# Kernel tuning notes

Hardware: AMD Instinct MI355X
Metric: run time of the kernel (lower is better)

## Reference

```python
import jax, jax.numpy as jnp
import numpy as np
from math import factorial, pi, sqrt

N_ATOMS = 4096
N_PAIRS = 49152
F = 16           # num_tensordense_features
NUM_RADIAL = 16  # basis num=16
NUM_SPECIES = 95
EMB_DIM = 32
CUTOFF = 5.0
LMAX = 4         # SelfAttention max_degree=4
NLM = 25
LMAX_B = 2       # basis max_degree=2 (also max_tensordense_degree)
NLM_B = 9

DEG9 = np.repeat(np.arange(3), [1, 3, 5])        # degree index of each lm, l<=2
DEG25 = np.repeat(np.arange(5), [1, 3, 5, 7, 9]) # degree index of each lm, l<=4


def real_sph(u, lmax):
    # real spherical harmonics (m = -l..l ordering, no Condon-Shortley), u: (...,3) unit vectors
    x, y, z = u[..., 0], u[..., 1], u[..., 2]
    phi = jnp.arctan2(y, x)
    ct = jnp.clip(z, -1.0, 1.0)
    st = jnp.sqrt(jnp.clip(1.0 - ct * ct, 0.0, 1.0))
    P = {(0, 0): jnp.ones_like(ct)}
    for m in range(1, lmax + 1):
        P[(m, m)] = -(2 * m - 1) * st * P[(m - 1, m - 1)]
    for m in range(0, lmax):
        P[(m + 1, m)] = (2 * m + 1) * ct * P[(m, m)]
    for m in range(0, lmax + 1):
        for l in range(m + 2, lmax + 1):
            P[(l, m)] = ((2 * l - 1) * ct * P[(l - 1, m)] - (l + m - 1) * P[(l - 2, m)]) / (l - m)
    outs = []
    for l in range(lmax + 1):
        for m in range(-l, l + 1):
            ma = abs(m)
            Nn = sqrt((2 * l + 1) / (4 * pi) * factorial(l - ma) / factorial(l + ma))
            cs = (-1.0) ** ma  # cancel Condon-Shortley in P
            if m == 0:
                Y = Nn * P[(l, 0)]
            elif m > 0:
                Y = sqrt(2.0) * Nn * cs * jnp.cos(m * phi) * P[(l, m)]
            else:
                Y = sqrt(2.0) * Nn * cs * jnp.sin(ma * phi) * P[(l, ma)]
            outs.append(Y)
    return jnp.stack(outs, axis=-1)


def _gaunt():
    # exact real Gaunt (CG-equivalent) coupling coefficients via Gauss-Legendre x uniform-phi quadrature
    nt, nph = 16, 32
    xs, ws = np.polynomial.legendre.leggauss(nt)
    phis = np.arange(nph) * (2 * np.pi / nph)
    ct = np.repeat(xs, nph); ph = np.tile(phis, nt)
    st = np.sqrt(np.clip(1.0 - ct ** 2, 0.0, 1.0))
    u = np.stack([st * np.cos(ph), st * np.sin(ph), ct], -1)
    w = np.repeat(ws, nph) * (2 * np.pi / nph)
    Y = np.asarray(real_sph(jnp.asarray(u, dtype=jnp.float32), LMAX))
    G = np.einsum('gi,gj,gk,g->ijk', Y, Y[:, :NLM_B], Y, w)
    G[np.abs(G) < 1e-6] = 0.0
    return G

_G = _gaunt()
G_ATT = jnp.asarray(_G, dtype=jnp.float32)                      # (25, 9, 25): feat x basis -> feat
G_TD = jnp.asarray(_G[:NLM_B, :, :NLM_B], dtype=jnp.float32)    # (9, 9, 9): TensorDense coupling


def pdense(x, W, deg):
    return jnp.einsum('plf,lfg->plg', x, W[deg])


def couple(xf, Bf, G):
    # equivariant tensor product  out[p,k,f] = sum_ij G[i,j,k] xf[p,i,f] Bf[p,j,f]
    u = jnp.einsum('pif,ijk->pjkf', xf, G)
    return jnp.einsum('pjf,pjkf->pkf', Bf, u)


def setup_inputs() -> dict:
    key = jax.random.key(0)
    ks = jax.random.split(key, 24)
    s = 1.0 / np.sqrt(F)
    inp = dict(
        atomic_numbers=jax.random.randint(ks[0], (N_ATOMS,), 0, NUM_SPECIES),
        neighbour_indices=jnp.stack([
            jax.random.randint(ks[1], (N_PAIRS,), 0, N_ATOMS),
            jax.random.randint(ks[2], (N_PAIRS,), 0, N_ATOMS)], axis=-1),
        neighbour_displacements=jax.random.normal(ks[3], (N_PAIRS, 3), dtype=jnp.float32) * 1.7,
        W_rad=jax.random.normal(ks[4], (NUM_SPECIES, NUM_RADIAL, F), dtype=jnp.float32) / np.sqrt(NUM_RADIAL),
        emb_table=jax.random.normal(ks[5], (NUM_SPECIES, EMB_DIM), dtype=jnp.float32),
        W_emb=jax.random.normal(ks[6], (EMB_DIM, F), dtype=jnp.float32) / np.sqrt(EMB_DIM),
        b_emb=jnp.zeros((F,), jnp.float32),
        td_W1=jax.random.normal(ks[7], (3, F, F), dtype=jnp.float32) * s,
        td_W2=jax.random.normal(ks[8], (3, F, F), dtype=jnp.float32) * s,
        td_W3=jax.random.normal(ks[9], (3, F, F), dtype=jnp.float32) * s,
        Wb1=jax.random.normal(ks[10], (NUM_RADIAL, F), dtype=jnp.float32) / np.sqrt(NUM_RADIAL),
        Wq1=jax.random.normal(ks[11], (5, F, F), dtype=jnp.float32) * s,
        Wk1=jax.random.normal(ks[12], (5, F, F), dtype=jnp.float32) * s,
        Wv1=jax.random.normal(ks[13], (5, F, F), dtype=jnp.float32) * s,
        Wo1=jax.random.normal(ks[14], (5, F, F), dtype=jnp.float32) * s,
        bo1=jnp.zeros((F,), jnp.float32),
        Wb2=jax.random.normal(ks[15], (NUM_RADIAL, F), dtype=jnp.float32) / np.sqrt(NUM_RADIAL),
        Wq2=jax.random.normal(ks[16], (5, F, F), dtype=jnp.float32) * s,
        Wk2=jax.random.normal(ks[17], (5, F, F), dtype=jnp.float32) * s,
        Wv2=jax.random.normal(ks[18], (5, F, F), dtype=jnp.float32) * s,
        Wo2=jax.random.normal(ks[19], (5, F, F), dtype=jnp.float32) * s,
        bo2=jnp.zeros((F,), jnp.float32),
    )
    return inp


def reference(atomic_numbers, neighbour_indices, neighbour_displacements,
              W_rad, emb_table, W_emb, b_emb, td_W1, td_W2, td_W3,
              Wb1, Wq1, Wk1, Wv1, Wo1, bo1, Wb2, Wq2, Wk2, Wv2, Wo2, bo2):
    dst = neighbour_indices[:, 0]   # idx_i
    src = neighbour_indices[:, 1]   # idx_j
    Zj = atomic_numbers[src]
    r = jnp.linalg.norm(neighbour_displacements, axis=-1)
    u = neighbour_displacements / jnp.maximum(r, 1e-9)[:, None]
    sh = real_sph(u, LMAX)          # (P, 25)
    sh_b = sh[:, :NLM_B]            # (P, 9)
    kk = jnp.arange(1, NUM_RADIAL + 1, dtype=jnp.float32)
    rb = jnp.sinc(kk[None, :] * r[:, None] / CUTOFF) * (r < CUTOFF)[:, None]  # sinc basis w/ cutoff
    # species-aware radial basis -> per-pair equivariant features (P, 9, F)
    y0 = jnp.einsum('pk,pkf->pf', rb, W_rad[Zj])
    y = sh_b[:, :, None] * y0[:, None, :]
    # TensorDense: dense -> CG tensor product -> dense (degrees <= 2)
    a = pdense(y, td_W1, DEG9)
    b = pdense(y, td_W2, DEG9)
    u9 = jnp.einsum('pif,ijk->pjkf', a, G_TD)
    tp = jnp.einsum('pjf,pjkf->pkf', b, u9)
    y = pdense(tp, td_W3, DEG9)
    # aggregate per-pair messages to atoms (segment mean), pad degrees to l<=4
    sums = jnp.zeros((N_ATOMS, NLM_B, F), y.dtype).at[dst].add(y)
    cnt = jnp.zeros((N_ATOMS,), y.dtype).at[dst].add(1.0)
    x = sums / jnp.maximum(cnt, 1.0)[:, None, None]
    x = jnp.pad(x, ((0, 0), (0, NLM - NLM_B), (0, 0)))  # (N, 25, F)
    # two segment self-attention layers over neighbour pairs
    for (Wb, Wq, Wk, Wv, Wo, bo) in ((Wb1, Wq1, Wk1, Wv1, Wo1, bo1), (Wb2, Wq2, Wk2, Wv2, Wo2, bo2)):
        Bf = sh_b[:, :, None] * (rb @ Wb)[:, None, :]   # projected pair basis (P, 9, F)
        q = pdense(x, Wq, DEG25)[dst]
        kf = couple(pdense(x, Wk, DEG25)[src], Bf, G_ATT)
        vf = couple(pdense(x, Wv, DEG25)[src], Bf, G_ATT)
        s = jnp.einsum('plf,plf->p', q, kf) / np.sqrt(NLM * F)
        m = jax.lax.stop_gradient(jnp.full((N_ATOMS,), -1e30, s.dtype).at[dst].max(s))
        e = jnp.exp(s - m[dst])
        den = jnp.zeros((N_ATOMS,), s.dtype).at[dst].add(e)
        alpha = e / (den[dst] + 1e-9)
        agg = jnp.zeros((N_ATOMS, NLM, F), x.dtype).at[dst].add(alpha[:, None, None] * vf)
        x = pdense(agg, Wo, DEG25)
        x = x.at[:, 0, :].add(bo)
    # embedding residual connection on the scalar (l=0) channel
    res = emb_table[atomic_numbers] @ W_emb + b_emb
    x = x.at[:, 0, :].add(res)
    return x
```

## Files before the change

### kernel.cpp

```cpp
#include <hip/hip_runtime.h>
#include <hip/hip_bf16.h>

#define NA 4096
#define NP 49152

typedef _Float16 f16;
typedef _Float16 h2 __attribute__((ext_vector_type(2)));
union U4H { uint4 u; f16 h[8]; h2 p[4]; };

__device__ __forceinline__ float fdot2(h2 a, h2 b, float c){
#if __has_builtin(__builtin_amdgcn_fdot2)
  return __builtin_amdgcn_fdot2(a, b, c, false);
#else
  return c + (float)a.x*(float)b.x + (float)a.y*(float)b.y;
#endif
}

constexpr int WS_Y     = 0;
constexpr int WS_G     = 12800;
constexpr int WS_NATT  = WS_G + 5632;
constexpr int WS_ATTW  = WS_NATT + 8;
constexpr int WS_ATTIJ = WS_ATTW + 1024;
constexpr int WS_TDOFS = WS_ATTIJ + 1024;
constexpr int WS_TDW   = WS_TDOFS + 16;
constexpr int WS_TDIJ  = WS_TDW + 512;
constexpr int WS_AOFS  = WS_TDIJ + 512;
constexpr int WS_SH    = WS_AOFS + 32;
constexpr int WS_RB    = WS_SH + NP*9;
constexpr int WS_S     = WS_RB + NP*16;
constexpr int WS_CCNT  = WS_S + NP;
constexpr int WS_COFF  = WS_CCNT + NA;
constexpr int WS_CCUR  = WS_COFF + NA + 8;
constexpr int WS_CLST  = WS_CCUR + NA;
constexpr int WS_XQ    = WS_CLST + NP;
constexpr int WS_XK    = WS_XQ + NA*400;
constexpr int WS_XV    = WS_XK + NA*400;
constexpr int WS_PVF   = WS_XV + NA*400;
constexpr int WS_WW    = WS_PVF + NP*128;
constexpr long long WS_END = (long long)WS_PVF + (long long)NP*256;

__device__ const float  GLX[16] = {
  -0.98940093499164993f, -0.94457502307323258f, -0.86563120238783174f, -0.75540440835500303f,
  -0.61787624440264375f, -0.45801677765722739f, -0.28160355077925891f, -0.09501250983763744f,
   0.09501250983763744f,  0.28160355077925891f,  0.45801677765722739f,  0.61787624440264375f,
   0.75540440835500303f,  0.86563120238783174f,  0.94457502307323258f,  0.98940093499164993f };
__device__ const double GLW[16] = {
  0.02715245941175409, 0.06225352393864789, 0.09515851168249278, 0.12462897125553387,
  0.14959598881657673, 0.16915651939500254, 0.18260341504492359, 0.18945061045506850,
  0.18945061045506850, 0.18260341504492359, 0.16915651939500254, 0.14959598881657673,
  0.12462897125553387, 0.09515851168249278, 0.06225352393864789, 0.02715245941175409 };

#define PI_D 3.14159265358979323846

__device__ __forceinline__ float scrub(float v){
  if(!(v == v)) return 0.f;
  return fminf(fmaxf(v, -1e30f), 1e30f);
}

__device__ void real_sph25(float ct, float phi, float* Y){
  float st = sqrtf(fmaxf(0.f, 1.f - ct*ct));
  float P[5][5];
  P[0][0] = 1.f;
  #pragma unroll
  for(int m=1;m<=4;m++) P[m][m] = -(2.f*m - 1.f)*st*P[m-1][m-1];
  #pragma unroll
  for(int m=0;m<4;m++) P[m+1][m] = (2.f*m + 1.f)*ct*P[m][m];
  #pragma unroll
  for(int m=0;m<=4;m++){
    #pragma unroll
    for(int l=m+2;l<=4;l++)
      P[l][m] = ((2.f*l - 1.f)*ct*P[l-1][m] - (float)(l+m-1)*P[l-2][m]) / (float)(l-m);
  }
  const double fact[9] = {1,1,2,6,24,120,720,5040,40320};
  int idx = 0;
  #pragma unroll
  for(int l=0;l<=4;l++){
    #pragma unroll
    for(int m=-l;m<=l;m++){
      int ma = (m < 0) ? -m : m;
      float Nn = (float)sqrt((2*l+1)/(4.0*PI_D)*fact[l-ma]/fact[l+ma]);
      float cs = (ma & 1) ? -1.f : 1.f;
      float v;
      if(m == 0)      v = Nn * P[l][0];
      else if(m > 0)  v = 1.4142135623730951f * Nn * cs * cosf(ma*phi) * P[l][ma];
      else            v = 1.4142135623730951f * Nn * cs * sinf(ma*phi) * P[l][ma];
      Y[idx++] = v;
    }
  }
}

__global__ __launch_bounds__(256) void kq_G(float* ws){
  __shared__ float Ysh[12800];
  int tid = threadIdx.x;
  for(int pt=tid; pt<512; pt+=256){
    float ct  = GLX[pt >> 5];
    float phi = (float)((pt & 31) * (2.0*PI_D/32.0));
    float Y[25];
    real_sph25(ct, phi, Y);
    #pragma unroll
    for(int i=0;i<25;i++) Ysh[pt*25 + i] = Y[i];
  }
  __syncthreads();
  int idx = blockIdx.x*256 + tid;
  int t = idx >> 3, chunk = idx & 7;
  if(t >= 5625) return;
  int k = t % 25, j = (t/25) % 9, i = t/225;
  double acc = 0.0;
  int g0 = chunk*64;
  #pragma unroll 4
  for(int g=g0; g<g0+64; g++){
    double w = GLW[g >> 5] * (2.0*PI_D/32.0);
    acc += w * (double)Ysh[g*25+i] * (double)Ysh[g*25+j] * (double)Ysh[g*25+k];
  }
  acc += __shfl_xor(acc, 1, 8);
  acc += __shfl_xor(acc, 2, 8);
  acc += __shfl_xor(acc, 4, 8);
  if(chunk == 0){
    if(fabs(acc) < 1e-6) acc = 0.0;
    ws[WS_G + (i*9+j)*25 + k] = (float)acc;
  }
}

__global__ __launch_bounds__(64) void kq_lists(float* ws){
  __shared__ float Gsh[5632];
  __shared__ int cA[25], cT[9], oA[26], oT[10];
  int t = threadIdx.x;
  for(int i=t; i<5625; i+=64) Gsh[i] = ws[WS_G + i];
  __syncthreads();
  const float* G = Gsh;
  if(t < 25){ int c=0; for(int i=0;i<25;i++) for(int j=0;j<9;j++) if(G[(i*9+j)*25+t] != 0.f) c++; cA[t]=c; }
  if(t < 9){  int c=0; for(int i=0;i<9;i++)  for(int j=0;j<9;j++) if(G[(i*9+j)*25+t] != 0.f) c++; cT[t]=c; }
  __syncthreads();
  if(t == 0){
    int s=0; for(int k=0;k<25;k++){ oA[k]=s; s+=cA[k]; } oA[25]=s;
    ((int*)ws)[WS_NATT] = s;
    s=0; for(int k=0;k<9;k++){ oT[k]=s; s+=cT[k]; } oT[9]=s;
  }
  __syncthreads();
  float* attw = ws + WS_ATTW; int* attij = (int*)ws + WS_ATTIJ;
  int* aofs = (int*)ws + WS_AOFS;
  if(t < 26) aofs[t] = oA[t] < 1024 ? oA[t] : 1024;
  if(t < 25){
    int pos = oA[t];
    for(int i=0;i<25;i++) for(int j=0;j<9;j++){
      float w = G[(i*9+j)*25+t];
      if(w != 0.f && pos < 1024){ attw[pos]=w; attij[pos] = i | (j<<5) | (t<<9); pos++; }
    }
  }
  float* tdw = ws + WS_TDW; int* tdij = (int*)ws + WS_TDIJ; int* tdofs = (int*)ws + WS_TDOFS;
  if(t < 9){
    int pos = oT[t];
    for(int i=0;i<9;i++) for(int j=0;j<9;j++){
      float w = G[(i*9+j)*25+t];
      if(w != 0.f && pos < 512){
        int li = (i==0)?0:(i<4)?1:2, lj = (j==0)?0:(j<4)?1:2;
        tdw[pos]=w; tdij[pos] = i | (j<<5) | (li<<10) | (lj<<12); pos++;
      }
    }
    tdofs[t] = oT[t];
    if(t == 0) tdofs[9] = oT[9];
  }
}

__global__ void k_pair(const float* disp, const int* nbr, float* ws){
  int p = blockIdx.x*256 + threadIdx.x;
  if(p >= NP) return;
  float dx = disp[3*p], dy = disp[3*p+1], dz = disp[3*p+2];
  float r = sqrtf(dx*dx + dy*dy + dz*dz);
  float inv = 1.f / fmaxf(r, 1e-9f);
  float ux = dx*inv, uy = dy*inv, uz = dz*inv;
  float sh[9];
  sh[0] = 0.28209479177387814f;
  sh[1] = 0.4886025119029199f * uy;
  sh[2] = 0.4886025119029199f * uz;
  sh[3] = 0.4886025119029199f * ux;
  sh[4] = 1.0925484305920792f * ux*uy;
  sh[5] = 1.0925484305920792f * uy*uz;
  sh[6] = 0.31539156525252005f * (3.f*uz*uz - 1.f);
  sh[7] = 1.0925484305920792f * ux*uz;
  sh[8] = 0.5462742152960396f * (ux*ux - uy*uy);
  #pragma unroll
  for(int i=0;i<9;i++) ws[WS_SH + p*9 + i] = scrub(sh[i]);
  float mask = (r < 5.f) ? 1.f : 0.f;
  #pragma unroll
  for(int k=1;k<=16;k++){
    float x  = (float)k * r * 0.2f;
    float px = 3.14159265358979323846f * x;
    float s  = (px < 1e-6f) ? 1.f : (sinf(px)/px);
    ws[WS_RB + p*16 + (k-1)] = scrub(s * mask);
  }
  atomicAdd((int*)ws + WS_CCNT + nbr[2*p], 1);
}

__global__ __launch_bounds__(1024) void k_scan(float* ws){
  __shared__ int part[1024];
  int t = threadIdx.x;
  const int* cnt = (const int*)ws + WS_CCNT;
  int v0 = cnt[4*t], v1 = cnt[4*t+1], v2 = cnt[4*t+2], v3 = cnt[4*t+3];
  part[t] = v0+v1+v2+v3;
  __syncthreads();
  for(int o=1; o<1024; o<<=1){
    int x = (t >= o) ? part[t-o] : 0;
    __syncthreads();
    part[t] += x;
    __syncthreads();
  }
  int base = (t > 0) ? part[t-1] : 0;
  int* offp = (int*)ws + WS_COFF;
  int* cur  = (int*)ws + WS_CCUR;
  offp[4*t]   = base;          cur[4*t]   = base;
  offp[4*t+1] = base+v0;       cur[4*t+1] = base+v0;
  offp[4*t+2] = base+v0+v1;    cur[4*t+2] = base+v0+v1;
  offp[4*t+3] = base+v0+v1+v2; cur[4*t+3] = base+v0+v1+v2;
  if(t == 1023) offp[4096] = part[1023];
}

__global__ void k_fill(const int* nbr, float* ws){
  int p = blockIdx.x*256 + threadIdx.x;
  if(p >= NP) return;
  int d = nbr[2*p];
  int pos = atomicAdd((int*)ws + WS_CCUR + d, 1);
  ((int*)ws)[WS_CLST + pos] = p;
}

__global__ __launch_bounds__(256) void k_ww(const float* Wrad, const float* W1,
                                            const float* W2, float* ws){
  int s = blockIdx.x;
  #pragma unroll
  for(int it=0; it<6; it++){
    int idx = threadIdx.x + 256*it;
    int w = idx / 768, r = idx % 768;
    int d = r / 256, r2 = r % 256, k = r2 / 16, g = r2 % 16;
    const float* Wsrc = (w == 0) ? W1 : W2;
    float acc = 0.f;
    #pragma unroll
    for(int fp=0; fp<16; fp++)
      acc += Wrad[(s*16+k)*16+fp] * Wsrc[(d*16+fp)*16+g];
    ws[WS_WW + ((size_t)(s*2+w)*16 + g)*48 + d*16 + k] = acc;
  }
}

__global__ __launch_bounds__(256) void k_td(const int* aZ, const int* nbr,
    const float* W3, float* ws){
  __shared__ float sh_s[16][9];
  __shared__ float S_s[16][88];
  __shared__ float tp_s[16][9][16];
  int tid = threadIdx.x, pl = tid >> 4, g = tid & 15;
  int sp = blockIdx.x*16 + pl;
  int p = ((const int*)ws)[WS_CLST + sp];
  int src = nbr[2*p+1];
  int Zj = aZ[src];
  {
    float4* S4 = (float4*)&S_s[0][0];
    for(int t0=tid; t0<352; t0+=256) S4[t0] = make_float4(0.f,0.f,0.f,0.f);
  }
  if(g < 9) sh_s[pl][g] = ws[WS_SH + p*9 + g];
  float rb[16];
  {
    const float4* rb4 = (const float4*)(ws + WS_RB + p*16);
    #pragma unroll
    for(int c=0;c<4;c++){
      float4 r = rb4[c];
      rb[4*c]=r.x; rb[4*c+1]=r.y; rb[4*c+2]=r.z; rb[4*c+3]=r.w;
    }
  }
  float A1[3], A2[3];
  {
    const float4* w1 = (const float4*)(ws + WS_WW + ((size_t)(Zj*2+0)*16+g)*48);
    const float4* w2 = (const float4*)(ws + WS_WW + ((size_t)(Zj*2+1)*16+g)*48);
    #pragma unroll
    for(int d=0; d<3; d++){
      float a1 = 0.f, a2 = 0.f;
      #pragma unroll
      for(int c=0;c<4;c++){
        float4 x1 = w1[d*4+c], x2 = w2[d*4+c];
        a1 += x1.x*rb[4*c] + x1.y*rb[4*c+1] + x1.z*rb[4*c+2] + x1.w*rb[4*c+3];
        a2 += x2.x*rb[4*c] + x2.y*rb[4*c+1] + x2.z*rb[4*c+2] + x2.w*rb[4*c+3];
      }
      A1[d] = a1; A2[d] = a2;
    }
  }
  __syncthreads();
  if(g < 9){
    const float* tdw = ws + WS_TDW;
    const int* tdij  = (const int*)ws + WS_TDIJ;
    const int* tdofs = (const int*)ws + WS_TDOFS;
    int e1 = tdofs[g+1];
    for(int e=tdofs[g]; e<e1; e++){
      float w = tdw[e]; int meta = tdij[e];
      int i = meta & 31, j = (meta>>5) & 15, li = (meta>>10) & 3, lj = (meta>>12) & 3;
      S_s[pl][g*9 + li*3 + lj] += w * sh_s[pl][i] * sh_s[pl][j];
    }
  }
  __syncthreads();
  float AA[9];
  #pragma unroll
  for(int li=0;li<3;li++)
    #pragma unroll
    for(int lj=0;lj<3;lj++) AA[li*3+lj] = A1[li]*A2[lj];
  #pragma unroll
  for(int k=0;k<9;k++){
    float tpv = 0.f;
    #pragma unroll
    for(int c=0;c<9;c++) tpv += S_s[pl][k*9+c] * AA[c];
    tp_s[pl][k][g] = tpv;
  }
  __syncthreads();
  float w3r[48];
  #pragma unroll
  for(int d=0;d<3;d++)
    #pragma unroll
    for(int f2=0;f2<16;f2++) w3r[d*16+f2] = W3[(d*16+f2)*16+g];
  float acc9[9];
  #pragma unroll
  for(int k=0;k<9;k++){
    int d = (k==0)?0:(k<4)?1:2;
    const float4* t4 = (const float4*)&tp_s[pl][k][0];
    float acc = 0.f;
    #pragma unroll
    for(int c=0;c<4;c++){
      float4 t = t4[c];
      acc += t.x*w3r[d*16+4*c] + t.y*w3r[d*16+4*c+1] + t.z*w3r[d*16+4*c+2] + t.w*w3r[d*16+4*c+3];
    }
    acc9[k] = scrub(acc);
  }
  f16* ptd = (f16*)(ws + WS_PVF) + (size_t)sp*256 + g*16;
  U4H u0, u1;
  #pragma unroll
  for(int j=0;j<8;j++) u0.h[j] = (f16)acc9[j];
  u1.h[0] = (f16)acc9[8];
  #pragma unroll
  for(int j=1;j<8;j++) u1.h[j] = (f16)0.f;
  *(uint4*)(ptd)     = u0.u;
  *(uint4*)(ptd + 8) = u1.u;
}

__global__ __launch_bounds__(256) void k_tdq(const float* Wq, const float* Wk,
                                             const float* Wv, float* ws){
  __shared__ float xsh[4][144];
  __shared__ float wq_sh[768], wk_sh[768], wv_sh[768];
  int tid = threadIdx.x, al = tid >> 6, lane = tid & 63;
  int a = blockIdx.x*4 + al;
  for(int t=tid; t<768; t+=256){ wq_sh[t]=Wq[t]; wk_sh[t]=Wk[t]; wv_sh[t]=Wv[t]; }
  const int* coff = (const int*)ws + WS_COFF;
  int off0 = coff[a], n = coff[a+1] - off0;
  const f16* base = (const f16*)(ws + WS_PVF);
  float acc[8] = {0,0,0,0,0,0,0,0};
  if(lane < 32){
    for(int t=0; t<n; t++){
      U4H u; u.u = *(const uint4*)(base + (size_t)(off0+t)*256 + lane*8);
      #pragma unroll
      for(int j=0;j<8;j++) acc[j] += (float)u.h[j];
    }
  }
  float invn = 1.f / fmaxf((float)n, 1.f);
  if(lane < 32){
    int gg = lane >> 1;
    #pragma unroll
    for(int j=0;j<8;j++){
      int k = (lane & 1)*8 + j;
      if(k < 9) xsh[al][k*16 + gg] = scrub(acc[j]*invn);
    }
  }
  __syncthreads();
  int g = lane & 15, q4 = lane >> 4;
  f16* qt = (f16*)(ws + WS_XQ) + (size_t)a*800 + g*32;
  f16* kt = (f16*)(ws + WS_XK) + (size_t)a*800 + g*32;
  f16* vt = (f16*)(ws + WS_XV) + (size_t)a*800 + g*32;
  for(int i=q4; i<9; i+=4){
    int l = (i==0)?0:(i<4)?1:2;
    float q=0.f, k2=0.f, v2=0.f;
    #pragma unroll
    for(int f2=0;f2<16;f2++){
      float xv = xsh[al][i*16+f2];
      q  += xv*wq_sh[(l*16+f2)*16+g];
      k2 += xv*wk_sh[(l*16+f2)*16+g];
      v2 += xv*wv_sh[(l*16+f2)*16+g];
    }
    qt[i] = (f16)q; kt[i] = (f16)k2; vt[i] = (f16)v2;
  }
}

template<int NI>
__global__ __launch_bounds__(128) void k_att(const int* nbr, const float* Wb, float* ws){
  __shared__ __align__(16) f16 Ml[8][840];
  __shared__ float sh_s[8][9];
  constexpr int NPAIR = NI/2;
  constexpr int TAIL  = NI-1;
  int tid = threadIdx.x, pl = tid >> 4, g = tid & 15;
  int sp = blockIdx.x*8 + pl;
  int p = ((const int*)ws)[WS_CLST + sp];
  {
    uint4 z; z.x=0; z.y=0; z.z=0; z.w=0;
    uint4* Mz = (uint4*)&Ml[0][0];
    for(int t0=tid; t0<840; t0+=128) Mz[t0] = z;
  }
  if(g < 9) sh_s[pl][g] = ws[WS_SH + p*9 + g];
  float wbreg[16];
  #pragma unroll
  for(int k=0;k<16;k++) wbreg[k] = Wb[k*16+g];
  __syncthreads();
  {
    const float* attw = ws + WS_ATTW;
    const int* attij  = (const int*)ws + WS_ATTIJ;
    const int* aofs   = (const int*)ws + WS_AOFS;
    for(int kr=g; kr<25; kr+=16){
      f16* Mrow = &Ml[pl][kr*32];
      int e = aofs[kr], e1 = aofs[kr+1];
      int meta = attij[e];
      int curi = meta & 31;
      float cur = 0.f;
      for(; e<e1; e++){
        meta = attij[e];
        int i2 = meta & 31;
        if(i2 != curi){ Mrow[curi] = (f16)cur; cur = 0.f; curi = i2; }
        cur += attw[e] * sh_s[pl][(meta>>5) & 15];
      }
      Mrow[curi] = (f16)cur;
    }
  }
  __syncthreads();
  int dst = nbr[2*p], src = nbr[2*p+1];
  float q_r[NI];
  {
    const f16* qt = (const f16*)(ws + WS_XQ) + (size_t)dst*800 + g*32;
    #pragma unroll
    for(int c=0;c<NPAIR/4;c++){
      U4H u; u.u = *(const uint4*)(qt + c*8);
      #pragma unroll
      for(int j=0;j<8;j++) q_r[c*8+j] = (float)u.h[j];
    }
    q_r[TAIL] = (float)qt[TAIL];
  }
  h2 xk2[NPAIR], xv2[NPAIR];
  float xkT, xvT;
  {
    const f16* kt = (const f16*)(ws + WS_XK) + (size_t)src*800 + g*32;
    const f16* vt = (const f16*)(ws + WS_XV) + (size_t)src*800 + g*32;
    #pragma unroll
    for(int c=0;c<NPAIR/4;c++){
      U4H uk; uk.u = *(const uint4*)(kt + c*8);
      U4H uv; uv.u = *(const uint4*)(vt + c*8);
      #pragma unroll
      for(int j=0;j<4;j++){ xk2[c*4+j] = uk.p[j]; xv2[c*4+j] = uv.p[j]; }
    }
    xkT = (float)kt[TAIL];
    xvT = (float)vt[TAIL];
  }
  float wbf;
  {
    const float4* rb4 = (const float4*)(ws + WS_RB + p*16);
    float acc = 0.f;
    #pragma unroll
    for(int c=0;c<4;c++){
      float4 r = rb4[c];
      acc += r.x*wbreg[4*c] + r.y*wbreg[4*c+1] + r.z*wbreg[4*c+2] + r.w*wbreg[4*c+3];
    }
    wbf = acc;
  }
  f16* pvf = (f16*)(ws + WS_PVF) + (size_t)sp*400;
  float sacc = 0.f;
  #pragma unroll
  for(int k=0;k<25;k++){
    const uint4* Mq = (const uint4*)&Ml[pl][k*32];
    float mT = (float)Ml[pl][k*32 + TAIL];
    float vv = 0.f, kf = 0.f;
    #pragma unroll
    for(int c=0;c<NPAIR/4;c++){
      U4H u; u.u = Mq[c];
      #pragma unroll
      for(int j=0;j<4;j++){
        vv = fdot2(u.p[j], xv2[c*4+j], vv);
        if(k < NI) kf = fdot2(u.p[j], xk2[c*4+j], kf);
      }
    }
    vv += mT * xvT;
    if(k < NI){
      kf += mT * xkT;
      sacc += q_r[k]*kf;
    }
    pvf[k*16 + g] = (f16)scrub(wbf*vv);
  }
  float sl = sacc;
  #pragma unroll
  for(int off=1; off<16; off<<=1) sl += __shfl_xor(sl, off, 16);
  if(g == 0) ws[WS_S + sp] = scrub(sl * 0.05f);
}

template<bool FINAL>
__global__ __launch_bounds__(256) void k_aggo(const float* Wo, const float* bo,
    const int* aZ, const float* emb, const float* Wemb, const float* bemb,
    const float* Wq, const float* Wk, const float* Wv, float* ws, float* out){
  __shared__ float xsh[4][400];
  __shared__ float wo_sh[1280];
  __shared__ float wq_sh[FINAL?4:1280], wk_sh[FINAL?4:1280], wv_sh[FINAL?4:1280];
  __shared__ float osh[FINAL?4:1600];
  int tid = threadIdx.x, al = tid >> 6, lane = tid & 63;
  int a = blockIdx.x*4 + al;
  for(int t=tid; t<1280; t+=256){
    wo_sh[t] = Wo[t];
    if(!FINAL){ wq_sh[t]=Wq[t]; wk_sh[t]=Wk[t]; wv_sh[t]=Wv[t]; }
  }
  const int* coff = (const int*)ws + WS_COFF;
  int off0 = coff[a], n = coff[a+1] - off0;
  float mx = -1e30f;
  for(int t=lane; t<n; t+=64) mx = fmaxf(mx, ws[WS_S + off0 + t]);
  #pragma unroll
  for(int off=1; off<64; off<<=1) mx = fmaxf(mx, __shfl_xor(mx, off));
  float den = 0.f;
  for(int t=lane; t<n; t+=64) den += expf(fminf(ws[WS_S + off0 + t] - mx, 0.f));
  #pragma unroll
  for(int off=1; off<64; off<<=1) den += __shfl_xor(den, off);
  float inv_den = 1.f / (den + 1e-9f);
  float acc[8] = {0,0,0,0,0,0,0,0};
  const f16* base = (const f16*)(ws + WS_PVF);
  for(int t=0; t<n; t++){
    float alpha = expf(fminf(ws[WS_S + off0 + t] - mx, 0.f)) * inv_den;
    if(lane < 50){
      U4H u; u.u = *(const uint4*)(base + (size_t)(off0+t)*400 + lane*8);
      #pragma unroll
      for(int j=0;j<8;j++) acc[j] += alpha * (float)u.h[j];
    }
  }
  if(lane < 50){
    #pragma unroll
    for(int j=0;j<8;j++) xsh[al][lane*8 + j] = scrub(acc[j]);
  }
  __syncthreads();
  int g = lane & 15, q4 = lane >> 4;
  for(int i=q4; i<25; i+=4){
    int l = (i==0)?0:(i<4)?1:(i<9)?2:(i<16)?3:4;
    float accv = 0.f;
    #pragma unroll
    for(int f2=0;f2<16;f2++) accv += xsh[al][i*16+f2]*wo_sh[(l*16+f2)*16+g];
    if(i == 0){
      accv += bo[g];
      if(FINAL){
        int Z = aZ[a];
        float res = bemb[g];
        #pragma unroll
        for(int e2=0;e2<32;e2++) res += emb[Z*32+e2]*Wemb[e2*16+g];
        accv += res;
      }
    }
    if(FINAL) out[a*400 + i*16 + g] = scrub(accv);
    else      osh[al*400 + i*16 + g] = scrub(accv);
  }
  if(!FINAL){
    __syncthreads();
    f16* qt = (f16*)(ws + WS_XQ) + (size_t)a*800 + g*32;
    f16* kt = (f16*)(ws + WS_XK) + (size_t)a*800 + g*32;
    f16* vt = (f16*)(ws + WS_XV) + (size_t)a*800 + g*32;
    for(int i=q4; i<25; i+=4){
      int l = (i==0)?0:(i<4)?1:(i<9)?2:(i<16)?3:4;
      float q=0.f, k2=0.f, v2=0.f;
      #pragma unroll
      for(int f2=0;f2<16;f2++){
        float xv = osh[al*400 + i*16 + f2];
        q  += xv*wq_sh[(l*16+f2)*16+g];
        k2 += xv*wk_sh[(l*16+f2)*16+g];
        v2 += xv*wv_sh[(l*16+f2)*16+g];
      }
      qt[i] = (f16)q; kt[i] = (f16)k2; vt[i] = (f16)v2;
    }
  }
}

extern "C" void kernel_launch(void* const* d_in, const int* in_sizes, int n_in,
                              void* d_out, int out_size, void* d_ws, size_t ws_size,
                              hipStream_t stream){
  (void)in_sizes; (void)n_in; (void)out_size;
  if(ws_size < (size_t)WS_END * sizeof(float)) return;
  float* ws = (float*)d_ws;
  const int* aZ  = (const int*)d_in[0];
  const int* nbr = (const int*)d_in[1];
  const float* disp = (const float*)d_in[2];
  const float* Wrad = (const float*)d_in[3];
  const float* emb  = (const float*)d_in[4];
  const float* Wemb = (const float*)d_in[5];
  const float* bemb = (const float*)d_in[6];
  const float* W1   = (const float*)d_in[7];
  const float* W2   = (const float*)d_in[8];
  const float* W3   = (const float*)d_in[9];
  const float* Wb1 = (const float*)d_in[10]; const float* Wq1 = (const float*)d_in[11];
  const float* Wk1 = (const float*)d_in[12]; const float* Wv1 = (const float*)d_in[13];
  const float* Wo1 = (const float*)d_in[14]; const float* bo1 = (const float*)d_in[15];
  const float* Wb2 = (const float*)d_in[16]; const float* Wq2 = (const float*)d_in[17];
  const float* Wk2 = (const float*)d_in[18]; const float* Wv2 = (const float*)d_in[19];
  const float* Wo2 = (const float*)d_in[20]; const float* bo2 = (const float*)d_in[21];

  kq_G<<<176,256,0,stream>>>(ws);
  kq_lists<<<1,64,0,stream>>>(ws);
  hipMemsetAsync(ws + WS_CCNT, 0, NA*sizeof(int), stream);
  k_pair<<<192,256,0,stream>>>(disp, nbr, ws);
  k_scan<<<1,1024,0,stream>>>(ws);
  k_fill<<<192,256,0,stream>>>(nbr, ws);
  k_ww<<<95,256,0,stream>>>(Wrad, W1, W2, ws);
  k_td<<<3072,256,0,stream>>>(aZ, nbr, W3, ws);
  k_tdq<<<1024,256,0,stream>>>(Wq1, Wk1, Wv1, ws);

  k_att<9><<<6144,128,0,stream>>>(nbr, Wb1, ws);
  k_aggo<false><<<1024,256,0,stream>>>(Wo1, bo1, aZ, emb, Wemb, bemb,
                                       Wq2, Wk2, Wv2, ws, nullptr);
  k_att<25><<<6144,128,0,stream>>>(nbr, Wb2, ws);
  k_aggo<true><<<1024,256,0,stream>>>(Wo2, bo2, aZ, emb, Wemb, bemb,
                                      nullptr, nullptr, nullptr, ws, (float*)d_out);
}
```

Measured before the change: 427.2 us.

## Store pair data in dst-sorted order and trim layer-1 attention coupling lists

Pair counting is split out of k_pair so the sorted pair order exists before spherical harmonics and radial basis are written. Those values, plus dst/src indices, are then stored at the sorted position, so k_td and k_att read contiguously instead of indirecting through the pair list and the neighbour array. A separate coupling list restricted to i<9 is built for the first attention layer, with a smaller shared-memory M tile. Wb is staged through shared memory instead of per-thread registers. This adds one extra kernel launch and an inverse-index scatter in k_fill.

```diff
diff --git a/kernel.cpp b/kernel.cpp
--- a/kernel.cpp
+++ b/kernel.cpp
@@ -16,7 +16,9 @@
 #endif
 }
 
-constexpr int WS_Y     = 0;
+constexpr int WS_AOFS9 = 64;
+constexpr int WS_ATTW9 = 128;
+constexpr int WS_ATTIJ9= WS_ATTW9 + 512;
 constexpr int WS_G     = 12800;
 constexpr int WS_NATT  = WS_G + 5632;
 constexpr int WS_ATTW  = WS_NATT + 8;
@@ -37,7 +39,10 @@
 constexpr int WS_XV    = WS_XK + NA*400;
 constexpr int WS_PVF   = WS_XV + NA*400;
 constexpr int WS_WW    = WS_PVF + NP*128;
-constexpr long long WS_END = (long long)WS_PVF + (long long)NP*256;
+constexpr int WS_PVFE  = WS_PVF + NP*256;
+constexpr int WS_INV   = WS_PVFE;
+constexpr int WS_DS    = WS_INV + NP;
+constexpr long long WS_END = (long long)WS_DS + 2*NP + 16;
 
 __device__ const float  GLX[16] = {
   -0.98940093499164993f, -0.94457502307323258f, -0.86563120238783174f, -0.75540440835500303f,
@@ -123,28 +128,38 @@
 
 __global__ __launch_bounds__(64) void kq_lists(float* ws){
   __shared__ float Gsh[5632];
-  __shared__ int cA[25], cT[9], oA[26], oT[10];
+  __shared__ int cA[25], cT[9], cA9[25], oA[26], oT[10], oA9[26];
   int t = threadIdx.x;
   for(int i=t; i<5625; i+=64) Gsh[i] = ws[WS_G + i];
   __syncthreads();
   const float* G = Gsh;
-  if(t < 25){ int c=0; for(int i=0;i<25;i++) for(int j=0;j<9;j++) if(G[(i*9+j)*25+t] != 0.f) c++; cA[t]=c; }
+  if(t < 25){
+    int c=0, c9=0;
+    for(int i=0;i<25;i++) for(int j=0;j<9;j++) if(G[(i*9+j)*25+t] != 0.f){ c++; if(i<9) c9++; }
+    cA[t]=c; cA9[t]=c9;
+  }
   if(t < 9){  int c=0; for(int i=0;i<9;i++)  for(int j=0;j<9;j++) if(G[(i*9+j)*25+t] != 0.f) c++; cT[t]=c; }
   __syncthreads();
   if(t == 0){
     int s=0; for(int k=0;k<25;k++){ oA[k]=s; s+=cA[k]; } oA[25]=s;
     ((int*)ws)[WS_NATT] = s;
+    s=0; for(int k=0;k<25;k++){ oA9[k]=s; s+=cA9[k]; } oA9[25]=s;
     s=0; for(int k=0;k<9;k++){ oT[k]=s; s+=cT[k]; } oT[9]=s;
   }
   __syncthreads();
-  float* attw = ws + WS_ATTW; int* attij = (int*)ws + WS_ATTIJ;
-  int* aofs = (int*)ws + WS_AOFS;
-  if(t < 26) aofs[t] = oA[t] < 1024 ? oA[t] : 1024;
+  float* attw = ws + WS_ATTW;  int* attij = (int*)ws + WS_ATTIJ;
+  float* attw9 = ws + WS_ATTW9; int* attij9 = (int*)ws + WS_ATTIJ9;
+  int* aofs  = (int*)ws + WS_AOFS;
+  int* aofs9 = (int*)ws + WS_AOFS9;
+  if(t < 26){ aofs[t] = oA[t] < 1024 ? oA[t] : 1024; aofs9[t] = oA9[t] < 512 ? oA9[t] : 512; }
   if(t < 25){
-    int pos = oA[t];
+    int pos = oA[t], pos9 = oA9[t];
     for(int i=0;i<25;i++) for(int j=0;j<9;j++){
       float w = G[(i*9+j)*25+t];
-      if(w != 0.f && pos < 1024){ attw[pos]=w; attij[pos] = i | (j<<5) | (t<<9); pos++; }
+      if(w != 0.f){
+        if(pos < 1024){ attw[pos]=w; attij[pos] = i | (j<<5) | (t<<9); pos++; }
+        if(i < 9 && pos9 < 512){ attw9[pos9]=w; attij9[pos9] = i | (j<<5) | (t<<9); pos9++; }
+      }
     }
   }
   float* tdw = ws + WS_TDW; int* tdij = (int*)ws + WS_TDIJ; int* tdofs = (int*)ws + WS_TDOFS;
@@ -162,9 +177,50 @@
   }
 }
 
-__global__ void k_pair(const float* disp, const int* nbr, float* ws){
+__global__ void k_cnt(const int* nbr, float* ws){
   int p = blockIdx.x*256 + threadIdx.x;
   if(p >= NP) return;
+  atomicAdd((int*)ws + WS_CCNT + nbr[2*p], 1);
+}
+
+__global__ __launch_bounds__(1024) void k_scan(float* ws){
+  __shared__ int part[1024];
+  int t = threadIdx.x;
+  const int* cnt = (const int*)ws + WS_CCNT;
+  int v0 = cnt[4*t], v1 = cnt[4*t+1], v2 = cnt[4*t+2], v3 = cnt[4*t+3];
+  part[t] = v0+v1+v2+v3;
+  __syncthreads();
+  for(int o=1; o<1024; o<<=1){
+    int x = (t >= o) ? part[t-o] : 0;
+    __syncthreads();
+    part[t] += x;
+    __syncthreads();
+  }
+  int base = (t > 0) ? part[t-1] : 0;
+  int* offp = (int*)ws + WS_COFF;
+  int* cur  = (int*)ws + WS_CCUR;
+  offp[4*t]   = base;          cur[4*t]   = base;
+  offp[4*t+1] = base+v0;       cur[4*t+1] = base+v0;
+  offp[4*t+2] = base+v0+v1;    cur[4*t+2] = base+v0+v1;
+  offp[4*t+3] = base+v0+v1+v2; cur[4*t+3] = base+v0+v1+v2;
+  if(t == 1023) offp[4096] = part[1023];
+}
+
+__global__ void k_fill(const int* nbr, float* ws){
+  int p = blockIdx.x*256 + threadIdx.x;
+  if(p >= NP) return;
+  int d = nbr[2*p], s = nbr[2*p+1];
+  int pos = atomicAdd((int*)ws + WS_CCUR + d, 1);
+  ((int*)ws)[WS_CLST + pos] = p;
+  ((int*)ws)[WS_INV + p] = pos;
+  ((int*)ws)[WS_DS + 2*pos]     = d;
+  ((int*)ws)[WS_DS + 2*pos + 1] = s;
+}
+
+__global__ void k_pair(const float* disp, float* ws){
+  int p = blockIdx.x*256 + threadIdx.x;
+  if(p >= NP) return;
+  int sp = ((const int*)ws)[WS_INV + p];
   float dx = disp[3*p], dy = disp[3*p+1], dz = disp[3*p+2];
   float r = sqrtf(dx*dx + dy*dy + dz*dz);
   float inv = 1.f / fmaxf(r, 1e-9f);
@@ -180,47 +236,19 @@
   sh[7] = 1.0925484305920792f * ux*uz;
   sh[8] = 0.5462742152960396f * (ux*ux - uy*uy);
   #pragma unroll
-  for(int i=0;i<9;i++) ws[WS_SH + p*9 + i] = scrub(sh[i]);
+  for(int i=0;i<9;i++) ws[WS_SH + sp*9 + i] = scrub(sh[i]);
   float mask = (r < 5.f) ? 1.f : 0.f;
+  float rbv[16];
   #pragma unroll
   for(int k=1;k<=16;k++){
     float x  = (float)k * r * 0.2f;
     float px = 3.14159265358979323846f * x;
     float s  = (px < 1e-6f) ? 1.f : (sinf(px)/px);
-    ws[WS_RB + p*16 + (k-1)] = scrub(s * mask);
-  }
-  atomicAdd((int*)ws + WS_CCNT + nbr[2*p], 1);
-}
-
-__global__ __launch_bounds__(1024) void k_scan(float* ws){
-  __shared__ int part[1024];
-  int t = threadIdx.x;
-  const int* cnt = (const int*)ws + WS_CCNT;
-  int v0 = cnt[4*t], v1 = cnt[4*t+1], v2 = cnt[4*t+2], v3 = cnt[4*t+3];
-  part[t] = v0+v1+v2+v3;
-  __syncthreads();
-  for(int o=1; o<1024; o<<=1){
-    int x = (t >= o) ? part[t-o] : 0;
-    __syncthreads();
-    part[t] += x;
-    __syncthreads();
-  }
-  int base = (t > 0) ? part[t-1] : 0;
-  int* offp = (int*)ws + WS_COFF;
-  int* cur  = (int*)ws + WS_CCUR;
-  offp[4*t]   = base;          cur[4*t]   = base;
-  offp[4*t+1] = base+v0;       cur[4*t+1] = base+v0;
-  offp[4*t+2] = base+v0+v1;    cur[4*t+2] = base+v0+v1;
-  offp[4*t+3] = base+v0+v1+v2; cur[4*t+3] = base+v0+v1+v2;
-  if(t == 1023) offp[4096] = part[1023];
-}
-
-__global__ void k_fill(const int* nbr, float* ws){
-  int p = blockIdx.x*256 + threadIdx.x;
-  if(p >= NP) return;
-  int d = nbr[2*p];
-  int pos = atomicAdd((int*)ws + WS_CCUR + d, 1);
-  ((int*)ws)[WS_CLST + pos] = p;
+    rbv[k-1] = scrub(s * mask);
+  }
+  float4* rb4 = (float4*)(ws + WS_RB + sp*16);
+  #pragma unroll
+  for(int c=0;c<4;c++) rb4[c] = make_float4(rbv[4*c], rbv[4*c+1], rbv[4*c+2], rbv[4*c+3]);
 }
 
 __global__ __launch_bounds__(256) void k_ww(const float* Wrad, const float* W1,
@@ -240,24 +268,22 @@
   }
 }
 
-__global__ __launch_bounds__(256) void k_td(const int* aZ, const int* nbr,
-    const float* W3, float* ws){
+__global__ __launch_bounds__(256) void k_td(const int* aZ, const float* W3, float* ws){
   __shared__ float sh_s[16][9];
   __shared__ float S_s[16][88];
   __shared__ float tp_s[16][9][16];
   int tid = threadIdx.x, pl = tid >> 4, g = tid & 15;
   int sp = blockIdx.x*16 + pl;
-  int p = ((const int*)ws)[WS_CLST + sp];
-  int src = nbr[2*p+1];
+  int src = ((const int*)ws)[WS_DS + 2*sp + 1];
   int Zj = aZ[src];
   {
     float4* S4 = (float4*)&S_s[0][0];
     for(int t0=tid; t0<352; t0+=256) S4[t0] = make_float4(0.f,0.f,0.f,0.f);
   }
-  if(g < 9) sh_s[pl][g] = ws[WS_SH + p*9 + g];
+  if(g < 9) sh_s[pl][g] = ws[WS_SH + sp*9 + g];
   float rb[16];
   {
-    const float4* rb4 = (const float4*)(ws + WS_RB + p*16);
+    const float4* rb4 = (const float4*)(ws + WS_RB + sp*16);
     #pragma unroll
     for(int c=0;c<4;c++){
       float4 r = rb4[c];
@@ -382,45 +408,48 @@
 }
 
 template<int NI>
-__global__ __launch_bounds__(128) void k_att(const int* nbr, const float* Wb, float* ws){
-  __shared__ __align__(16) f16 Ml[8][840];
+__global__ __launch_bounds__(128) void k_att(const float* Wb, float* ws){
+  constexpr int MROWH = (NI == 9) ? 16 : 32;
+  constexpr int PLSTR = (NI == 9) ? 408 : 840;
+  __shared__ __align__(16) f16 Ml[8][PLSTR];
   __shared__ float sh_s[8][9];
+  __shared__ float wb_sh[256];
   constexpr int NPAIR = NI/2;
   constexpr int TAIL  = NI-1;
   int tid = threadIdx.x, pl = tid >> 4, g = tid & 15;
   int sp = blockIdx.x*8 + pl;
-  int p = ((const int*)ws)[WS_CLST + sp];
   {
     uint4 z; z.x=0; z.y=0; z.z=0; z.w=0;
     uint4* Mz = (uint4*)&Ml[0][0];
-    for(int t0=tid; t0<840; t0+=128) Mz[t0] = z;
-  }
-  if(g < 9) sh_s[pl][g] = ws[WS_SH + p*9 + g];
-  float wbreg[16];
-  #pragma unroll
-  for(int k=0;k<16;k++) wbreg[k] = Wb[k*16+g];
-  __syncthreads();
-  {
-    const float* attw = ws + WS_ATTW;
-    const int* attij  = (const int*)ws + WS_ATTIJ;
-    const int* aofs   = (const int*)ws + WS_AOFS;
+    for(int t0=tid; t0<PLSTR; t0+=128) Mz[t0] = z;
+  }
+  for(int t0=tid; t0<256; t0+=128) wb_sh[t0] = Wb[t0];
+  if(g < 9) sh_s[pl][g] = ws[WS_SH + sp*9 + g];
+  __syncthreads();
+  {
+    const float* attw = ws + (NI==9 ? WS_ATTW9 : WS_ATTW);
+    const int* attij  = (const int*)ws + (NI==9 ? WS_ATTIJ9 : WS_ATTIJ);
+    const int* aofs   = (const int*)ws + (NI==9 ? WS_AOFS9 : WS_AOFS);
     for(int kr=g; kr<25; kr+=16){
-      f16* Mrow = &Ml[pl][kr*32];
+      f16* Mrow = &Ml[pl][kr*MROWH];
       int e = aofs[kr], e1 = aofs[kr+1];
-      int meta = attij[e];
-      int curi = meta & 31;
-      float cur = 0.f;
-      for(; e<e1; e++){
-        meta = attij[e];
-        int i2 = meta & 31;
-        if(i2 != curi){ Mrow[curi] = (f16)cur; cur = 0.f; curi = i2; }
-        cur += attw[e] * sh_s[pl][(meta>>5) & 15];
+      if(e < e1){
+        int meta = attij[e];
+        int curi = meta & 31;
+        float cur = 0.f;
+        for(; e<e1; e++){
+          meta = attij[e];
+          int i2 = meta & 31;
+          if(i2 != curi){ Mrow[curi] = (f16)cur; cur = 0.f; curi = i2; }
+          cur += attw[e] * sh_s[pl][(meta>>5) & 15];
+        }
+        Mrow[curi] = (f16)cur;
       }
-      Mrow[curi] = (f16)cur;
-    }
-  }
-  __syncthreads();
-  int dst = nbr[2*p], src = nbr[2*p+1];
+    }
+  }
+  __syncthreads();
+  int dst = ((const int*)ws)[WS_DS + 2*sp];
+  int src = ((const int*)ws)[WS_DS + 2*sp + 1];
   float q_r[NI];
   {
     const f16* qt = (const f16*)(ws + WS_XQ) + (size_t)dst*800 + g*32;
@@ -449,12 +478,13 @@
   }
   float wbf;
   {
-    const float4* rb4 = (const float4*)(ws + WS_RB + p*16);
+    const float4* rb4 = (const float4*)(ws + WS_RB + sp*16);
     float acc = 0.f;
     #pragma unroll
     for(int c=0;c<4;c++){
       float4 r = rb4[c];
-      acc += r.x*wbreg[4*c] + r.y*wbreg[4*c+1] + r.z*wbreg[4*c+2] + r.w*wbreg[4*c+3];
+      acc += r.x*wb_sh[(4*c)*16+g] + r.y*wb_sh[(4*c+1)*16+g]
+           + r.z*wb_sh[(4*c+2)*16+g] + r.w*wb_sh[(4*c+3)*16+g];
     }
     wbf = acc;
   }
@@ -462,8 +492,8 @@
   float sacc = 0.f;
   #pragma unroll
   for(int k=0;k<25;k++){
-    const uint4* Mq = (const uint4*)&Ml[pl][k*32];
-    float mT = (float)Ml[pl][k*32 + TAIL];
+    const uint4* Mq = (const uint4*)&Ml[pl][k*MROWH];
+    float mT = (float)Ml[pl][k*MROWH + TAIL];
     float vv = 0.f, kf = 0.f;
     #pragma unroll
     for(int c=0;c<NPAIR/4;c++){
@@ -592,17 +622,18 @@
   kq_G<<<176,256,0,stream>>>(ws);
   kq_lists<<<1,64,0,stream>>>(ws);
   hipMemsetAsync(ws + WS_CCNT, 0, NA*sizeof(int), stream);
-  k_pair<<<192,256,0,stream>>>(disp, nbr, ws);
+  k_cnt<<<192,256,0,stream>>>(nbr, ws);
   k_scan<<<1,1024,0,stream>>>(ws);
   k_fill<<<192,256,0,stream>>>(nbr, ws);
+  k_pair<<<192,256,0,stream>>>(disp, ws);
   k_ww<<<95,256,0,stream>>>(Wrad, W1, W2, ws);
-  k_td<<<3072,256,0,stream>>>(aZ, nbr, W3, ws);
+  k_td<<<3072,256,0,stream>>>(aZ, W3, ws);
   k_tdq<<<1024,256,0,stream>>>(Wq1, Wk1, Wv1, ws);
 
-  k_att<9><<<6144,128,0,stream>>>(nbr, Wb1, ws);
+  k_att<9><<<6144,128,0,stream>>>(Wb1, ws);
   k_aggo<false><<<1024,256,0,stream>>>(Wo1, bo1, aZ, emb, Wemb, bemb,
                                        Wq2, Wk2, Wv2, ws, nullptr);
-  k_att<25><<<6144,128,0,stream>>>(nbr, Wb2, ws);
+  k_att<25><<<6144,128,0,stream>>>(Wb2, ws);
   k_aggo<true><<<1024,256,0,stream>>>(Wo2, bo2, aZ, emb, Wemb, bemb,
                                       nullptr, nullptr, nullptr, ws, (float*)d_out);
 }
```

New measurement: 400.1 us. 1.07x faster.
